# Optimization experiments

Measured on AMD Instinct MI355X. Metric: run time of the kernel, lower is better.

The kernel has to match this reference:

```python
import jax, jax.numpy as jnp
import numpy as np

E, H = 512, 8
D = E // H  # head_dim = 64
NEG = jnp.finfo(jnp.float32).min


def setup_inputs() -> dict:
    key = jax.random.key(0)
    ks = jax.random.split(key, 12)
    s = 0.02
    return {
        "image": jax.random.normal(ks[0], (16, 197, E), jnp.float32),
        "text": jax.random.normal(ks[1], (64, 30, E), jnp.float32),
        "text_mask": jax.random.randint(ks[2], (64, 29), 0, 2).astype(bool),
        "Wq": jax.random.normal(ks[3], (D, D), jnp.float32) * s,
        "Wk": jax.random.normal(ks[4], (D, D), jnp.float32) * s,
        "Wv": jax.random.normal(ks[5], (D, D), jnp.float32) * s,
        "W_out": jax.random.normal(ks[6], (E, E), jnp.float32) * s,
        "b_out": jnp.zeros((E,), jnp.float32),
        "Wtv": jax.random.normal(ks[7], (D, D), jnp.float32) * s,
        "W_out_text": jax.random.normal(ks[8], (E, E), jnp.float32) * s,
        "b_out_text": jnp.zeros((E,), jnp.float32),
    }


def reference(image, text, text_mask, Wq, Wk, Wv, W_out, b_out, Wtv, W_out_text, b_out_text):
    I, Q, _ = image.shape
    T, K, _ = text.shape
    img = image.reshape(I, Q, H, D)
    txt = text.reshape(T, K, H, D)
    # per-head linear projections (torch Linear: y = x @ W.T)
    q = img @ Wq.T            # [I,Q,H,D]
    k = txt @ Wk.T            # [T,K,H,D]
    v = txt @ Wv.T            # [T,K,H,D]
    # cross-batch bidirectional attention energy [I,T,H,Q,K]
    energy = jnp.einsum('tkhd,iqhd->ithqk', k, q)
    # cls_present: pad mask with True at front along K
    mask = jnp.pad(text_mask, ((0, 0), (1, 0)), constant_values=True)  # [T,K]
    energy = jnp.where(mask[None, :, None, None, :], energy, NEG)
    scaled = energy / jnp.sqrt(jnp.float32(E))
    attention = jax.nn.softmax(scaled, axis=-1)       # over k (i2t)
    text_attention = jax.nn.softmax(scaled, axis=-2)  # over q (t2i)
    # i2t branch: [I,T,Q,H,D] -> [I,T,Q,E]
    out = jnp.einsum('ithqk,tkhd->itqhd', attention, v).reshape(I, T, Q, E)
    out = out @ W_out.T + b_out
    out = out.mean(axis=2)  # mean pool over image tokens -> [I,T,E]
    # t2i branch: [I,T,K,H,D] -> [I,T,K,E]
    tv = img @ Wtv.T  # [I,Q,H,D]
    out_text = jnp.einsum('ithqk,iqhd->itkhd', text_attention, tv).reshape(I, T, K, E)
    out_text = out_text @ W_out_text.T + b_out_text
    out_text = out_text.mean(axis=2)  # mean pool over text tokens -> [I,T,E]
    return (out, out_text, attention, text_attention)
```

## Files before the change

### kernel.cpp

```cpp
#include <hip/hip_runtime.h>
#include <hip/hip_bf16.h>
#include <cstdint>

#define I_ 16
#define T_ 64
#define Q_ 197
#define K_ 30
#define H_ 8
#define D_ 64
#define E_ 512

typedef float f32x2 __attribute__((ext_vector_type(2)));
typedef float f32x4 __attribute__((ext_vector_type(4)));
typedef short bf16x8 __attribute__((ext_vector_type(8)));

static constexpr float INV_SQRT_E = 0.044194173824159216f;
static constexpr float C197 = 1.0f / 197.0f;
static constexpr int   QK = Q_ * K_;

#define OFF_QBF   0
#define OFF_KBF   806912
#define OFF_VBF   1298432
#define OFF_TVBF  1789952
#define OFF_ASUM  2596864
#define OFF_TASUM 2842624
#define OFF_PBF   4456448
#define OFF_WBF   4980736

__device__ inline short f2bs(float x) { __hip_bfloat16 h = __float2bfloat16(x); return *reinterpret_cast<short*>(&h); }
__device__ inline float bs2f(short s) { __hip_bfloat16 h = *reinterpret_cast<__hip_bfloat16*>(&s); return __bfloat162float(h); }

__global__ __launch_bounds__(512) void proj_kernel(
    const float* __restrict__ image, const float* __restrict__ text,
    const float* __restrict__ Wq, const float* __restrict__ Wk,
    const float* __restrict__ Wv, const float* __restrict__ Wtv,
    const float* __restrict__ W_out, const float* __restrict__ W_out_text,
    float* __restrict__ ws)
{
  const int NQ4 = (I_ * Q_) / 4;
  const int NT4 = (T_ * K_) / 4;
  int bb = blockIdx.x;
  int tid = threadIdx.x;

  if (bb >= NQ4 + 2 * NT4 + NQ4) {
    int row0 = (bb - (NQ4 + 2 * NT4 + NQ4)) * 4;
    __hip_bfloat16* Wb = (__hip_bfloat16*)(ws + OFF_WBF);
    const float* src = (row0 < 512) ? (W_out + row0 * E_) : (W_out_text + (row0 - 512) * E_);
    #pragma unroll
    for (int rr = 0; rr < 4; ++rr)
      Wb[(size_t)(row0 + rr) * E_ + tid] = __float2bfloat16(src[rr * E_ + tid]);
    return;
  }

  const float* X; const float* W; int row0; int mode;
  if (bb < NQ4)             { X = image; W = Wq;  row0 = bb * 4;               mode = 0; }
  else if (bb < NQ4 + NT4)  { X = text;  W = Wk;  row0 = (bb - NQ4) * 4;       mode = 1; }
  else if (bb < NQ4 + 2*NT4){ X = text;  W = Wv;  row0 = (bb - NQ4 - NT4) * 4; mode = 2; }
  else                      { X = image; W = Wtv; row0 = (bb - NQ4 - 2*NT4)*4; mode = 3; }

  __shared__ float s_x[4][E_];
  __shared__ float s_w[D_][D_ + 1];
  for (int idx = tid; idx < D_ * D_; idx += 512) s_w[idx >> 6][idx & 63] = W[idx];
  #pragma unroll
  for (int rr = 0; rr < 4; ++rr) s_x[rr][tid] = X[(size_t)(row0 + rr) * E_ + tid];
  __syncthreads();

  int h = tid >> 6, dout = tid & 63;
  float a0 = 0.f, a1 = 0.f, a2 = 0.f, a3 = 0.f;
  #pragma unroll
  for (int d = 0; d < D_; ++d) {
    float w = s_w[dout][d];
    a0 = fmaf(s_x[0][h * 64 + d], w, a0);
    a1 = fmaf(s_x[1][h * 64 + d], w, a1);
    a2 = fmaf(s_x[2][h * 64 + d], w, a2);
    a3 = fmaf(s_x[3][h * 64 + d], w, a3);
  }
  static const int offs[4] = { OFF_QBF, OFF_KBF, OFF_VBF, OFF_TVBF };
  __hip_bfloat16* Y = (__hip_bfloat16*)(ws + offs[mode]);
  Y[(size_t)(row0 + 0) * E_ + tid] = __float2bfloat16(a0);
  Y[(size_t)(row0 + 1) * E_ + tid] = __float2bfloat16(a1);
  Y[(size_t)(row0 + 2) * E_ + tid] = __float2bfloat16(a2);
  Y[(size_t)(row0 + 3) * E_ + tid] = __float2bfloat16(a3);
}

__global__ __launch_bounds__(256, 8) void attn_kernel(
    const __hip_bfloat16* __restrict__ qbf, const __hip_bfloat16* __restrict__ kbf,
    const int* __restrict__ text_mask,
    float* __restrict__ attn_out, float* __restrict__ tattn_out,
    float* __restrict__ A_sum, float* __restrict__ TA_sum)
{
  int b = blockIdx.x;
  int h = b & 7, t = (b >> 3) & 63, i = b >> 9;
  int tid = threadIdx.x;
  int w = tid >> 6, lane = tid & 63;
  int lr = lane & 15, lg = lane >> 4;

  __shared__ __align__(16) float s_stage[4][480];
  __shared__ float s_cd[4][32];
  __shared__ float s_ca[4][32];
  __shared__ float s_invd[32];

  int m0 = (lr == 0) ? 1 : text_mask[t * (K_ - 1) + lr - 1];
  int m1 = (lr < 14) ? text_mask[t * (K_ - 1) + 15 + lr] : 0;

  const __hip_bfloat16* qb = qbf + ((size_t)(i * Q_) * H_ + h) * D_;
  const __hip_bfloat16* kb = kbf + ((size_t)(t * K_) * H_ + h) * D_;

  const bf16x8* bp0 = (const bf16x8*)(kb + (size_t)lr * (H_ * D_) + lg * 8);
  const bf16x8* bp1 = (const bf16x8*)(kb + (size_t)(16 + lr) * (H_ * D_) + lg * 8);
  bf16x8 b00 = bp0[0], b01 = bp0[4];
  bf16x8 b10 = bp1[0], b11 = bp1[4];

  float* abase = attn_out  + (size_t)b * QK;
  float* tbase = tattn_out + (size_t)b * QK;

  float cd0 = 0.f, cd1 = 0.f, ca0 = 0.f, ca1 = 0.f;
  bf16x8 epk[4];

  #pragma unroll
  for (int j = 0; j < 4; ++j) {
    int mt = w + 4 * j;
    epk[j] = bf16x8{0, 0, 0, 0, 0, 0, 0, 0};
    if (mt < 13) {
      const bf16x8* ap = (const bf16x8*)(qb + (size_t)(mt * 16 + lr) * (H_ * D_) + lg * 8);
      bf16x8 a0 = ap[0], a1 = ap[4];
      f32x4 acc0 = {0.f, 0.f, 0.f, 0.f}, acc1 = {0.f, 0.f, 0.f, 0.f};
      acc0 = __builtin_amdgcn_mfma_f32_16x16x32_bf16(a0, b00, acc0, 0, 0, 0);
      acc0 = __builtin_amdgcn_mfma_f32_16x16x32_bf16(a1, b01, acc0, 0, 0, 0);
      acc1 = __builtin_amdgcn_mfma_f32_16x16x32_bf16(a0, b10, acc1, 0, 0, 0);
      acc1 = __builtin_amdgcn_mfma_f32_16x16x32_bf16(a1, b11, acc1, 0, 0, 0);
      int row0 = mt * 16 + lg * 4;
      float v0[4], v1[4], iv[4];
      #pragma unroll
      for (int r = 0; r < 4; ++r) {
        bool vr = (row0 + r) < Q_;
        v0[r] = (vr && m0) ? __expf(acc0[r] * INV_SQRT_E) : 0.f;
        v1[r] = (vr && m1) ? __expf(acc1[r] * INV_SQRT_E) : 0.f;
      }
      #pragma unroll
      for (int r = 0; r < 4; ++r) {
        float s = v0[r] + v1[r];
        s += __shfl_xor(s, 1);
        s += __shfl_xor(s, 2);
        s += __shfl_xor(s, 4);
        s += __shfl_xor(s, 8);
        iv[r] = ((row0 + r) < Q_ && s > 0.f) ? (1.0f / s) : 0.f;
        cd0 += v0[r]; ca0 += v0[r] * iv[r];
        cd1 += v1[r]; ca1 += v1[r] * iv[r];
      }
      #pragma unroll
      for (int r = 0; r < 4; ++r) {
        int rl = lg * 4 + r;
        s_stage[w][rl * K_ + lr] = v0[r] * iv[r];
        if (lr < 14) s_stage[w][rl * K_ + 16 + lr] = v1[r] * iv[r];
      }
      epk[j] = bf16x8{ f2bs(v0[0]), f2bs(v0[1]), f2bs(v0[2]), f2bs(v0[3]),
                       f2bs(v1[0]), f2bs(v1[1]), f2bs(v1[2]), f2bs(v1[3]) };
      const int nstore = (mt < 12) ? 240 : 75;
      #pragma unroll
      for (int it = 0; it < 4; ++it) {
        int idx = it * 64 + lane;
        if (idx < nstore) {
          f32x2 a2 = *(const f32x2*)&s_stage[w][2 * idx];
          *(f32x2*)(abase + mt * 480 + 2 * idx) = a2;
        }
      }
    }
  }

  cd0 += __shfl_xor(cd0, 16); cd0 += __shfl_xor(cd0, 32);
  ca0 += __shfl_xor(ca0, 16); ca0 += __shfl_xor(ca0, 32);
  cd1 += __shfl_xor(cd1, 16); cd1 += __shfl_xor(cd1, 32);
  ca1 += __shfl_xor(ca1, 16); ca1 += __shfl_xor(ca1, 32);
  if (lane < 16) {
    s_cd[w][lr] = cd0; s_cd[w][lr + 16] = cd1;
    s_ca[w][lr] = ca0; s_ca[w][lr + 16] = ca1;
  }
  __syncthreads();

  if (tid < 32) {
    int col = tid;
    float dsum = (s_cd[0][col] + s_cd[1][col]) + (s_cd[2][col] + s_cd[3][col]);
    float pa   = (s_ca[0][col] + s_ca[1][col]) + (s_ca[2][col] + s_ca[3][col]);
    int mc = (col == 0) ? 1 : (col < K_ ? text_mask[t * (K_ - 1) + col - 1] : 0);
    s_invd[col] = (mc && dsum > 0.f) ? (1.0f / dsum) : 0.f;
    if (col < K_) A_sum[(size_t)b * K_ + col] = pa;
  }
  __syncthreads();

  float invd0 = s_invd[lr];
  float invd1 = s_invd[16 + lr];
  float* ta_base = TA_sum + (size_t)b * Q_;

  #pragma unroll
  for (int j = 0; j < 4; ++j) {
    int mt = w + 4 * j;
    if (mt < 13) {
      int row0 = mt * 16 + lg * 4;
      float tvA[4], tvB[4];
      #pragma unroll
      for (int r = 0; r < 4; ++r) {
        float eA = bs2f(epk[j][r]);
        float eB = bs2f(epk[j][4 + r]);
        tvA[r] = m0 ? eA * invd0 : C197;
        tvB[r] = m1 ? eB * invd1 : C197;
        int rl = lg * 4 + r;
        s_stage[w][rl * K_ + lr] = tvA[r];
        if (lr < 14) s_stage[w][rl * K_ + 16 + lr] = tvB[r];
      }
      #pragma unroll
      for (int r = 0; r < 4; ++r) {
        float ta = tvA[r] + ((lr < 14) ? tvB[r] : 0.f);
        ta += __shfl_xor(ta, 1);
        ta += __shfl_xor(ta, 2);
        ta += __shfl_xor(ta, 4);
        ta += __shfl_xor(ta, 8);
        if (lr == 0 && (row0 + r) < Q_) ta_base[row0 + r] = ta;
      }
      const int nstore = (mt < 12) ? 240 : 75;
      #pragma unroll
      for (int it = 0; it < 4; ++it) {
        int idx = it * 64 + lane;
        if (idx < nstore) {
          f32x2 t2 = *(const f32x2*)&s_stage[w][2 * idx];
          *(f32x2*)(tbase + mt * 480 + 2 * idx) = t2;
        }
      }
    }
  }
}

__global__ __launch_bounds__(512) void pool_fused_kernel(
    const float* __restrict__ A_sum, const float* __restrict__ TA_sum,
    const __hip_bfloat16* __restrict__ vbf, const __hip_bfloat16* __restrict__ tvbf,
    __hip_bfloat16* __restrict__ Pbf)
{
  int bt = blockIdx.x;
  int t = bt & 63;
  int i = bt >> 6;
  int tid = threadIdx.x;
  int h = tid >> 6, d = tid & 63;
  __shared__ float s_A[H_ * K_];
  __shared__ float s_TA[H_ * Q_];
  if (tid < H_ * K_) s_A[tid] = A_sum[(size_t)bt * H_ * K_ + tid];
  for (int idx = tid; idx < H_ * Q_; idx += 512) s_TA[idx] = TA_sum[(size_t)bt * H_ * Q_ + idx];
  __syncthreads();

  {
    float a0 = 0.f, a1 = 0.f;
    #pragma unroll
    for (int kk = 0; kk < K_; kk += 2) {
      a0 = fmaf(s_A[h * K_ + kk],
                __bfloat162float(vbf[((size_t)(t * K_ + kk)     * H_ + h) * D_ + d]), a0);
      a1 = fmaf(s_A[h * K_ + kk + 1],
                __bfloat162float(vbf[((size_t)(t * K_ + kk + 1) * H_ + h) * D_ + d]), a1);
    }
    Pbf[(size_t)bt * E_ + tid] = __float2bfloat16((a0 + a1) * C197);
  }

  {
    float a0 = 0.f, a1 = 0.f, a2 = 0.f, a3 = 0.f;
    int qq = 0;
    for (; qq + 4 <= Q_; qq += 4) {
      a0 = fmaf(s_TA[h * Q_ + qq + 0],
                __bfloat162float(tvbf[((size_t)(i * Q_ + qq + 0) * H_ + h) * D_ + d]), a0);
      a1 = fmaf(s_TA[h * Q_ + qq + 1],
                __bfloat162float(tvbf[((size_t)(i * Q_ + qq + 1) * H_ + h) * D_ + d]), a1);
      a2 = fmaf(s_TA[h * Q_ + qq + 2],
                __bfloat162float(tvbf[((size_t)(i * Q_ + qq + 2) * H_ + h) * D_ + d]), a2);
      a3 = fmaf(s_TA[h * Q_ + qq + 3],
                __bfloat162float(tvbf[((size_t)(i * Q_ + qq + 3) * H_ + h) * D_ + d]), a3);
    }
    for (; qq < Q_; ++qq)
      a0 = fmaf(s_TA[h * Q_ + qq],
                __bfloat162float(tvbf[((size_t)(i * Q_ + qq) * H_ + h) * D_ + d]), a0);
    Pbf[(size_t)(1024 + bt) * E_ + tid] = __float2bfloat16(((a0 + a1) + (a2 + a3)) * (1.0f / 30.0f));
  }
}

__global__ __launch_bounds__(256) void outproj_mfma_kernel(
    const __hip_bfloat16* __restrict__ Pbf, const __hip_bfloat16* __restrict__ Wbf,
    const float* __restrict__ b_out, const float* __restrict__ b_out_text,
    float* __restrict__ out)
{
  int mt = blockIdx.x;
  int z = (mt >= 64);
  int tid = threadIdx.x;
  int w = tid >> 6, lane = tid & 63;
  int lr = lane & 15, lg = lane >> 4;

  const __hip_bfloat16* A = Pbf + (size_t)(mt * 16 + lr) * E_ + lg * 8;
  const __hip_bfloat16* B = Wbf + (size_t)(z * 512) * E_;
  f32x4 acc[8] = {};
  for (int ks = 0; ks < 16; ++ks) {
    bf16x8 a = *(const bf16x8*)(A + ks * 32);
    #pragma unroll
    for (int nt = 0; nt < 8; ++nt) {
      int n0 = w * 128 + nt * 16;
      bf16x8 bv = *(const bf16x8*)(B + (size_t)(n0 + lr) * E_ + ks * 32 + lg * 8);
      acc[nt] = __builtin_amdgcn_mfma_f32_16x16x32_bf16(a, bv, acc[nt], 0, 0, 0);
    }
  }
  const float* bias = z ? b_out_text : b_out;
  int row0 = mt * 16 + lg * 4;
  #pragma unroll
  for (int nt = 0; nt < 8; ++nt) {
    int n = w * 128 + nt * 16 + lr;
    float bv = bias[n];
    #pragma unroll
    for (int r = 0; r < 4; ++r)
      out[(size_t)(row0 + r) * E_ + n] = acc[nt][r] + bv;
  }
}

extern "C" void kernel_launch(void* const* d_in, const int* in_sizes, int n_in,
                              void* d_out, int out_size, void* d_ws, size_t ws_size,
                              hipStream_t stream)
{
  const float* image      = (const float*)d_in[0];
  const float* text       = (const float*)d_in[1];
  const int*   tmask      = (const int*)d_in[2];
  const float* Wq         = (const float*)d_in[3];
  const float* Wk         = (const float*)d_in[4];
  const float* Wv         = (const float*)d_in[5];
  const float* W_out      = (const float*)d_in[6];
  const float* b_out      = (const float*)d_in[7];
  const float* Wtv        = (const float*)d_in[8];
  const float* W_out_text = (const float*)d_in[9];
  const float* b_out_text = (const float*)d_in[10];

  float* out = (float*)d_out;
  float* ws  = (float*)d_ws;

  const __hip_bfloat16* qbf  = (const __hip_bfloat16*)(ws + OFF_QBF);
  const __hip_bfloat16* kbf  = (const __hip_bfloat16*)(ws + OFF_KBF);
  const __hip_bfloat16* vbf  = (const __hip_bfloat16*)(ws + OFF_VBF);
  const __hip_bfloat16* tvbf = (const __hip_bfloat16*)(ws + OFF_TVBF);
  float* Asum  = ws + OFF_ASUM;
  float* TAsum = ws + OFF_TASUM;
  __hip_bfloat16* Pbf = (__hip_bfloat16*)(ws + OFF_PBF);
  __hip_bfloat16* Wbf = (__hip_bfloat16*)(ws + OFF_WBF);

  float* attn    = out + (size_t)2 * I_ * T_ * E_;
  float* tattn   = attn + (size_t)I_ * T_ * H_ * Q_ * K_;

  const int NQ4 = (I_ * Q_) / 4, NT4 = (T_ * K_) / 4;
  proj_kernel<<<NQ4 + 2 * NT4 + NQ4 + 256, 512, 0, stream>>>(
      image, text, Wq, Wk, Wv, Wtv, W_out, W_out_text, ws);
  attn_kernel<<<I_ * T_ * H_, 256, 0, stream>>>(qbf, kbf, tmask, attn, tattn, Asum, TAsum);
  pool_fused_kernel<<<I_ * T_, 512, 0, stream>>>(Asum, TAsum, vbf, tvbf, Pbf);
  outproj_mfma_kernel<<<128, 256, 0, stream>>>(Pbf, Wbf, b_out, b_out_text, out);
}
```

Before: 189.5 us.

## Split attention kernel into reduction pass and recompute-and-store expand pass

The fused attention kernel is split in two. The first kernel computes softmax row and column normalisers plus pooled sums and writes them to workspace. The second kernel recomputes the QK energies with MFMA and streams both attention tensors to memory using those normalisers. This drops the bf16 packing of exponentials and the block barriers from the store-heavy phase, and lowers register pressure there. The cost is recomputing QK^T and exp, plus an extra launch and small workspace reads and writes.

```diff
diff --git a/kernel.cpp b/kernel.cpp
--- a/kernel.cpp
+++ b/kernel.cpp
@@ -26,9 +26,8 @@
 #define OFF_TASUM 2842624
 #define OFF_PBF   4456448
 #define OFF_WBF   4980736
-
-__device__ inline short f2bs(float x) { __hip_bfloat16 h = __float2bfloat16(x); return *reinterpret_cast<short*>(&h); }
-__device__ inline float bs2f(short s) { __hip_bfloat16 h = *reinterpret_cast<__hip_bfloat16*>(&s); return __bfloat162float(h); }
+#define OFF_IVR   5242880
+#define OFF_IVD   6946816
 
 __global__ __launch_bounds__(512) void proj_kernel(
     const float* __restrict__ image, const float* __restrict__ text,
@@ -83,10 +82,10 @@
   Y[(size_t)(row0 + 3) * E_ + tid] = __float2bfloat16(a3);
 }
 
-__global__ __launch_bounds__(256, 8) void attn_kernel(
+__global__ __launch_bounds__(256, 8) void attn_reduce_kernel(
     const __hip_bfloat16* __restrict__ qbf, const __hip_bfloat16* __restrict__ kbf,
     const int* __restrict__ text_mask,
-    float* __restrict__ attn_out, float* __restrict__ tattn_out,
+    float* __restrict__ invrow_o, float* __restrict__ invd_o,
     float* __restrict__ A_sum, float* __restrict__ TA_sum)
 {
   int b = blockIdx.x;
@@ -95,7 +94,6 @@
   int w = tid >> 6, lane = tid & 63;
   int lr = lane & 15, lg = lane >> 4;
 
-  __shared__ __align__(16) float s_stage[4][480];
   __shared__ float s_cd[4][32];
   __shared__ float s_ca[4][32];
   __shared__ float s_invd[32];
@@ -111,16 +109,127 @@
   bf16x8 b00 = bp0[0], b01 = bp0[4];
   bf16x8 b10 = bp1[0], b11 = bp1[4];
 
+  float cd0 = 0.f, cd1 = 0.f, ca0 = 0.f, ca1 = 0.f;
+  f32x4 e0[4], e1[4];
+
+  float* ivr_base = invrow_o + (size_t)b * 208;
+
+  #pragma unroll
+  for (int j = 0; j < 4; ++j) {
+    int mt = w + 4 * j;
+    e0[j] = f32x4{0.f, 0.f, 0.f, 0.f};
+    e1[j] = f32x4{0.f, 0.f, 0.f, 0.f};
+    if (mt < 13) {
+      const bf16x8* ap = (const bf16x8*)(qb + (size_t)(mt * 16 + lr) * (H_ * D_) + lg * 8);
+      bf16x8 a0 = ap[0], a1 = ap[4];
+      f32x4 acc0 = {0.f, 0.f, 0.f, 0.f}, acc1 = {0.f, 0.f, 0.f, 0.f};
+      acc0 = __builtin_amdgcn_mfma_f32_16x16x32_bf16(a0, b00, acc0, 0, 0, 0);
+      acc0 = __builtin_amdgcn_mfma_f32_16x16x32_bf16(a1, b01, acc0, 0, 0, 0);
+      acc1 = __builtin_amdgcn_mfma_f32_16x16x32_bf16(a0, b10, acc1, 0, 0, 0);
+      acc1 = __builtin_amdgcn_mfma_f32_16x16x32_bf16(a1, b11, acc1, 0, 0, 0);
+      int row0 = mt * 16 + lg * 4;
+      #pragma unroll
+      for (int r = 0; r < 4; ++r) {
+        bool vr = (row0 + r) < Q_;
+        e0[j][r] = (vr && m0) ? __expf(acc0[r] * INV_SQRT_E) : 0.f;
+        e1[j][r] = (vr && m1) ? __expf(acc1[r] * INV_SQRT_E) : 0.f;
+      }
+      #pragma unroll
+      for (int r = 0; r < 4; ++r) {
+        float s = e0[j][r] + e1[j][r];
+        s += __shfl_xor(s, 1);
+        s += __shfl_xor(s, 2);
+        s += __shfl_xor(s, 4);
+        s += __shfl_xor(s, 8);
+        float iv = ((row0 + r) < Q_ && s > 0.f) ? (1.0f / s) : 0.f;
+        if (lr == 0) ivr_base[row0 + r] = iv;
+        cd0 += e0[j][r]; ca0 += e0[j][r] * iv;
+        cd1 += e1[j][r]; ca1 += e1[j][r] * iv;
+      }
+    }
+  }
+
+  cd0 += __shfl_xor(cd0, 16); cd0 += __shfl_xor(cd0, 32);
+  ca0 += __shfl_xor(ca0, 16); ca0 += __shfl_xor(ca0, 32);
+  cd1 += __shfl_xor(cd1, 16); cd1 += __shfl_xor(cd1, 32);
+  ca1 += __shfl_xor(ca1, 16); ca1 += __shfl_xor(ca1, 32);
+  if (lane < 16) {
+    s_cd[w][lr] = cd0; s_cd[w][lr + 16] = cd1;
+    s_ca[w][lr] = ca0; s_ca[w][lr + 16] = ca1;
+  }
+  __syncthreads();
+
+  if (tid < 32) {
+    int col = tid;
+    float dsum = (s_cd[0][col] + s_cd[1][col]) + (s_cd[2][col] + s_cd[3][col]);
+    float pa   = (s_ca[0][col] + s_ca[1][col]) + (s_ca[2][col] + s_ca[3][col]);
+    int mc = (col == 0) ? 1 : (col < K_ ? text_mask[t * (K_ - 1) + col - 1] : 0);
+    float ivd = (mc && dsum > 0.f) ? (1.0f / dsum) : 0.f;
+    s_invd[col] = ivd;
+    invd_o[(size_t)b * 32 + col] = ivd;
+    if (col < K_) A_sum[(size_t)b * K_ + col] = pa;
+  }
+  __syncthreads();
+
+  float invd0 = s_invd[lr];
+  float invd1 = s_invd[16 + lr];
+  float* ta_base = TA_sum + (size_t)b * Q_;
+
+  #pragma unroll
+  for (int j = 0; j < 4; ++j) {
+    int mt = w + 4 * j;
+    if (mt < 13) {
+      int row0 = mt * 16 + lg * 4;
+      #pragma unroll
+      for (int r = 0; r < 4; ++r) {
+        float tvA = m0 ? e0[j][r] * invd0 : C197;
+        float tvB = (lr < 14) ? (m1 ? e1[j][r] * invd1 : C197) : 0.f;
+        float ta = tvA + tvB;
+        ta += __shfl_xor(ta, 1);
+        ta += __shfl_xor(ta, 2);
+        ta += __shfl_xor(ta, 4);
+        ta += __shfl_xor(ta, 8);
+        if (lr == 0 && (row0 + r) < Q_) ta_base[row0 + r] = ta;
+      }
+    }
+  }
+}
+
+__global__ __launch_bounds__(256, 8) void attn_expand_kernel(
+    const __hip_bfloat16* __restrict__ qbf, const __hip_bfloat16* __restrict__ kbf,
+    const int* __restrict__ text_mask,
+    const float* __restrict__ invrow_i, const float* __restrict__ invd_i,
+    float* __restrict__ attn_out, float* __restrict__ tattn_out)
+{
+  int b = blockIdx.x;
+  int h = b & 7, t = (b >> 3) & 63, i = b >> 9;
+  int tid = threadIdx.x;
+  int w = tid >> 6, lane = tid & 63;
+  int lr = lane & 15, lg = lane >> 4;
+
+  __shared__ __align__(16) float s_stage[4][480];
+
+  int m0 = (lr == 0) ? 1 : text_mask[t * (K_ - 1) + lr - 1];
+  int m1 = (lr < 14) ? text_mask[t * (K_ - 1) + 15 + lr] : 0;
+
+  const __hip_bfloat16* qb = qbf + ((size_t)(i * Q_) * H_ + h) * D_;
+  const __hip_bfloat16* kb = kbf + ((size_t)(t * K_) * H_ + h) * D_;
+
+  const bf16x8* bp0 = (const bf16x8*)(kb + (size_t)lr * (H_ * D_) + lg * 8);
+  const bf16x8* bp1 = (const bf16x8*)(kb + (size_t)(16 + lr) * (H_ * D_) + lg * 8);
+  bf16x8 b00 = bp0[0], b01 = bp0[4];
+  bf16x8 b10 = bp1[0], b11 = bp1[4];
+
+  float invd0 = invd_i[(size_t)b * 32 + lr];
+  float invd1 = invd_i[(size_t)b * 32 + 16 + lr];
+  const float* ivr_base = invrow_i + (size_t)b * 208;
+
   float* abase = attn_out  + (size_t)b * QK;
   float* tbase = tattn_out + (size_t)b * QK;
 
-  float cd0 = 0.f, cd1 = 0.f, ca0 = 0.f, ca1 = 0.f;
-  bf16x8 epk[4];
-
   #pragma unroll
   for (int j = 0; j < 4; ++j) {
     int mt = w + 4 * j;
-    epk[j] = bf16x8{0, 0, 0, 0, 0, 0, 0, 0};
     if (mt < 13) {
       const bf16x8* ap = (const bf16x8*)(qb + (size_t)(mt * 16 + lr) * (H_ * D_) + lg * 8);
       bf16x8 a0 = ap[0], a1 = ap[4];
@@ -136,17 +245,7 @@
         bool vr = (row0 + r) < Q_;
         v0[r] = (vr && m0) ? __expf(acc0[r] * INV_SQRT_E) : 0.f;
         v1[r] = (vr && m1) ? __expf(acc1[r] * INV_SQRT_E) : 0.f;
-      }
-      #pragma unroll
-      for (int r = 0; r < 4; ++r) {
-        float s = v0[r] + v1[r];
-        s += __shfl_xor(s, 1);
-        s += __shfl_xor(s, 2);
-        s += __shfl_xor(s, 4);
-        s += __shfl_xor(s, 8);
-        iv[r] = ((row0 + r) < Q_ && s > 0.f) ? (1.0f / s) : 0.f;
-        cd0 += v0[r]; ca0 += v0[r] * iv[r];
-        cd1 += v1[r]; ca1 += v1[r] * iv[r];
+        iv[r] = ivr_base[row0 + r];
       }
       #pragma unroll
       for (int r = 0; r < 4; ++r) {
@@ -154,8 +253,6 @@
         s_stage[w][rl * K_ + lr] = v0[r] * iv[r];
         if (lr < 14) s_stage[w][rl * K_ + 16 + lr] = v1[r] * iv[r];
       }
-      epk[j] = bf16x8{ f2bs(v0[0]), f2bs(v0[1]), f2bs(v0[2]), f2bs(v0[3]),
-                       f2bs(v1[0]), f2bs(v1[1]), f2bs(v1[2]), f2bs(v1[3]) };
       const int nstore = (mt < 12) ? 240 : 75;
       #pragma unroll
       for (int it = 0; it < 4; ++it) {
@@ -165,59 +262,12 @@
           *(f32x2*)(abase + mt * 480 + 2 * idx) = a2;
         }
       }
-    }
-  }
-
-  cd0 += __shfl_xor(cd0, 16); cd0 += __shfl_xor(cd0, 32);
-  ca0 += __shfl_xor(ca0, 16); ca0 += __shfl_xor(ca0, 32);
-  cd1 += __shfl_xor(cd1, 16); cd1 += __shfl_xor(cd1, 32);
-  ca1 += __shfl_xor(ca1, 16); ca1 += __shfl_xor(ca1, 32);
-  if (lane < 16) {
-    s_cd[w][lr] = cd0; s_cd[w][lr + 16] = cd1;
-    s_ca[w][lr] = ca0; s_ca[w][lr + 16] = ca1;
-  }
-  __syncthreads();
-
-  if (tid < 32) {
-    int col = tid;
-    float dsum = (s_cd[0][col] + s_cd[1][col]) + (s_cd[2][col] + s_cd[3][col]);
-    float pa   = (s_ca[0][col] + s_ca[1][col]) + (s_ca[2][col] + s_ca[3][col]);
-    int mc = (col == 0) ? 1 : (col < K_ ? text_mask[t * (K_ - 1) + col - 1] : 0);
-    s_invd[col] = (mc && dsum > 0.f) ? (1.0f / dsum) : 0.f;
-    if (col < K_) A_sum[(size_t)b * K_ + col] = pa;
-  }
-  __syncthreads();
-
-  float invd0 = s_invd[lr];
-  float invd1 = s_invd[16 + lr];
-  float* ta_base = TA_sum + (size_t)b * Q_;
-
-  #pragma unroll
-  for (int j = 0; j < 4; ++j) {
-    int mt = w + 4 * j;
-    if (mt < 13) {
-      int row0 = mt * 16 + lg * 4;
-      float tvA[4], tvB[4];
-      #pragma unroll
-      for (int r = 0; r < 4; ++r) {
-        float eA = bs2f(epk[j][r]);
-        float eB = bs2f(epk[j][4 + r]);
-        tvA[r] = m0 ? eA * invd0 : C197;
-        tvB[r] = m1 ? eB * invd1 : C197;
+      #pragma unroll
+      for (int r = 0; r < 4; ++r) {
         int rl = lg * 4 + r;
-        s_stage[w][rl * K_ + lr] = tvA[r];
-        if (lr < 14) s_stage[w][rl * K_ + 16 + lr] = tvB[r];
-      }
-      #pragma unroll
-      for (int r = 0; r < 4; ++r) {
-        float ta = tvA[r] + ((lr < 14) ? tvB[r] : 0.f);
-        ta += __shfl_xor(ta, 1);
-        ta += __shfl_xor(ta, 2);
-        ta += __shfl_xor(ta, 4);
-        ta += __shfl_xor(ta, 8);
-        if (lr == 0 && (row0 + r) < Q_) ta_base[row0 + r] = ta;
-      }
-      const int nstore = (mt < 12) ? 240 : 75;
+        s_stage[w][rl * K_ + lr] = m0 ? v0[r] * invd0 : C197;
+        if (lr < 14) s_stage[w][rl * K_ + 16 + lr] = m1 ? v1[r] * invd1 : C197;
+      }
       #pragma unroll
       for (int it = 0; it < 4; ++it) {
         int idx = it * 64 + lane;
@@ -340,6 +390,8 @@
   float* TAsum = ws + OFF_TASUM;
   __hip_bfloat16* Pbf = (__hip_bfloat16*)(ws + OFF_PBF);
   __hip_bfloat16* Wbf = (__hip_bfloat16*)(ws + OFF_WBF);
+  float* ivr  = ws + OFF_IVR;
+  float* ivd  = ws + OFF_IVD;
 
   float* attn    = out + (size_t)2 * I_ * T_ * E_;
   float* tattn   = attn + (size_t)I_ * T_ * H_ * Q_ * K_;
@@ -347,7 +399,8 @@
   const int NQ4 = (I_ * Q_) / 4, NT4 = (T_ * K_) / 4;
   proj_kernel<<<NQ4 + 2 * NT4 + NQ4 + 256, 512, 0, stream>>>(
       image, text, Wq, Wk, Wv, Wtv, W_out, W_out_text, ws);
-  attn_kernel<<<I_ * T_ * H_, 256, 0, stream>>>(qbf, kbf, tmask, attn, tattn, Asum, TAsum);
+  attn_reduce_kernel<<<I_ * T_ * H_, 256, 0, stream>>>(qbf, kbf, tmask, ivr, ivd, Asum, TAsum);
+  attn_expand_kernel<<<I_ * T_ * H_, 256, 0, stream>>>(qbf, kbf, tmask, ivr, ivd, attn, tattn);
   pool_fused_kernel<<<I_ * T_, 512, 0, stream>>>(Asum, TAsum, vbf, tvbf, Pbf);
   outproj_mfma_kernel<<<128, 256, 0, stream>>>(Pbf, Wbf, b_out, b_out_text, out);
 }
```

Measured after the change: 353.4 us. 86.5% more time.
